# Performance work log

Hardware: AMD Instinct MI355X
Metric: run time of the kernel (lower is better)

Reference implementation:

```python
import jax, jax.numpy as jnp
import numpy as np

B, N, D, E = 4, 2048, 1024, 4
H = 4 * D  # expert hidden (mult=4)


def setup_inputs() -> dict:
    key = jax.random.key(0)
    ks = jax.random.split(key, 8)
    std = 0.02
    return {
        "x": jax.random.normal(ks[0], (B, N, D), jnp.float32),
        "W_slot": jax.random.normal(ks[1], (E * D, D), jnp.float32) * std,
        "u_slot": jax.random.normal(ks[2], (D,), jnp.float32),
        "sigma_slot": jnp.ones((1,), jnp.float32),
        "W1": jax.random.normal(ks[3], (E, H, D), jnp.float32) * std,
        "b1": jnp.zeros((E, H), jnp.float32),
        "u1": jax.random.normal(ks[4], (E, D), jnp.float32),
        "sig1": jnp.ones((E,), jnp.float32),
        "W2": jax.random.normal(ks[5], (E, D, H), jnp.float32) * std,
        "b2": jnp.zeros((E, D), jnp.float32),
        "u2": jax.random.normal(ks[6], (E, H), jnp.float32),
        "sig2": jnp.ones((E,), jnp.float32),
    }


def _sn_weight(W, u, sigma):
    # One power-iteration step (no_grad in torch -> stop_gradient), then
    # sigma_spec = v^T W u'; weight = W / sigma_spec * learnable sigma.
    v = W @ u
    v = jax.lax.stop_gradient(v / jnp.linalg.norm(v))
    u2 = W.T @ v
    u2 = jax.lax.stop_gradient(u2 / jnp.linalg.norm(u2))
    s = jnp.einsum('c,cd,d->', v, W, u2)
    return W * (sigma / s)


def reference(x, W_slot, u_slot, sigma_slot, W1, b1, u1, sig1, W2, b2, u2, sig2):
    b, n, d = x.shape
    e = W1.shape[0]
    s = n // e  # slots per expert; n divisible by e -> no padding, no mask

    # dynamic slot embeddings from consecutive-segment means
    Wsl = _sn_weight(W_slot, u_slot, sigma_slot[0])          # [e*d, d]
    xm = x.reshape(b, s, e, d).mean(axis=2)                   # [b, s, d]
    slot_embeds = (xm @ Wsl.T).reshape(b, s, e, d)
    slot_embeds = slot_embeds.transpose(0, 2, 1, 3)           # [b, e, s, d]

    logits = jnp.einsum('bnd,besd->bnes', x, slot_embeds)     # [b, n, e, s]
    dispatch = jax.nn.softmax(logits, axis=1)                 # softmax over n
    combine = jax.nn.softmax(logits.reshape(b, n, e * s), axis=-1)

    slots = jnp.einsum('bnd,bnes->ebsd', x, dispatch)         # [e, b, s, d]

    # per-expert FFN with spectral-normed weights (vectorized over experts)
    W1n = jax.vmap(_sn_weight)(W1, u1, sig1)                  # [e, H, d]
    W2n = jax.vmap(_sn_weight)(W2, u2, sig2)                  # [e, d, H]
    h = jax.nn.gelu(jnp.einsum('ebsd,ehd->ebsh', slots, W1n) + b1[:, None, None, :],
                    approximate=False)
    y = jnp.einsum('ebsh,edh->ebsd', h, W2n) + b2[:, None, None, :]

    out = y.transpose(1, 0, 2, 3).reshape(b, e * s, d)        # [b, e*s, d]
    return jnp.einsum('bsd,bns->bnd', out, combine)           # [b, n, d]
```

## Files before the change

### kernel.cpp

```cpp
#include <hip/hip_runtime.h>
#include <hip/hip_bf16.h>
#include <math.h>

constexpr int CB  = 4;
constexpr int CN  = 2048;
constexpr int CD  = 1024;
constexpr int CE  = 4;
constexpr int CS  = 512;
constexpr int CH  = 4096;
constexpr int CES = 2048;

typedef unsigned short u16;
typedef unsigned int   u32;
typedef __bf16 bf16x8 __attribute__((ext_vector_type(8)));
typedef float  f32x4  __attribute__((ext_vector_type(4)));

__device__ __forceinline__ u16 f2bf(float x) {
  u32 u = __float_as_uint(x);
  u = (u + 0x7FFF + ((u >> 16) & 1)) >> 16;
  return (u16)u;
}

__device__ __forceinline__ void gl2lds16(const void* g, void* l) {
  __builtin_amdgcn_global_load_lds(
      (const __attribute__((address_space(1))) void*)g,
      (__attribute__((address_space(3))) void*)l, 16, 0, 0);
}

__device__ __forceinline__ void xcd_swz(int& bx, int& by, int& bz) {
  u32 gx = gridDim.x, gy = gridDim.y;
  u32 w = blockIdx.x + gx * (blockIdx.y + gy * blockIdx.z);
  u32 nwg = gx * gy * gridDim.z;
  u32 q = nwg >> 3;
  u32 wg = (w & 7) * q + (w >> 3);
  bx = wg % gx;
  u32 r = wg / gx;
  by = r % gy;
  bz = r / gy;
}


__global__ __launch_bounds__(256) void gemv_rows_k(const float* __restrict__ W,
    const float* __restrict__ u, float* __restrict__ t1, int M, int K, int ustride) {
  int bi = blockIdx.y;
  int row = blockIdx.x * 4 + (threadIdx.x >> 6);
  int lane = threadIdx.x & 63;
  const float* Wr = W + ((long)bi * M + row) * K;
  const float* ub = u + (long)bi * ustride;
  float s = 0.f;
  for (int k = lane; k < K; k += 64) s += Wr[k] * ub[k];
#pragma unroll
  for (int off = 32; off; off >>= 1) s += __shfl_down(s, off, 64);
  if (lane == 0) t1[bi * M + row] = s;
}

__global__ __launch_bounds__(256) void gemv_cols_k(const float* __restrict__ W,
    const float* __restrict__ t1, float* __restrict__ t2,
    u16* __restrict__ bh, u16* __restrict__ bl, int M, int K) {
  int bi = blockIdx.z;
  int k = blockIdx.x * 256 + threadIdx.x;
  int m0 = blockIdx.y * 256;
  const float* Wb = W + (long)bi * M * K;
  const float* tb = t1 + bi * M;
  u16* bhb = bh + (long)bi * M * K;
  u16* blb = bl ? bl + (long)bi * M * K : nullptr;
  float s = 0.f;
#pragma unroll 4
  for (int m = 0; m < 256; m++) {
    long idx = (long)(m0 + m) * K + k;
    float w = Wb[idx];
    s += w * tb[m0 + m];
    u16 h = f2bf(w);
    bhb[idx] = h;
    if (blb) blb[idx] = f2bf(w - __uint_as_float((u32)h << 16));
  }
  atomicAdd(&t2[bi * K + k], s);
}

__global__ __launch_bounds__(256) void scale_all_k(
    const float* __restrict__ t1s, const float* __restrict__ t2s,
    const float* __restrict__ t1a, const float* __restrict__ t2a,
    const float* __restrict__ t1b, const float* __restrict__ t2b,
    const float* __restrict__ sigs, const float* __restrict__ sig1,
    const float* __restrict__ sig2, float* __restrict__ scales) {
  int bi = blockIdx.x;
  const float *t1, *t2; float sg; float* o; int M, K;
  if (bi == 0)      { t1 = t1s;                 t2 = t2s;                 sg = sigs[0];     o = scales + 0;      M = 4096; K = 1024; }
  else if (bi < 5)  { int e = bi - 1; t1 = t1a + e * 4096; t2 = t2a + e * 1024; sg = sig1[e]; o = scales + 1 + e; M = 4096; K = 1024; }
  else              { int e = bi - 5; t1 = t1b + e * 1024; t2 = t2b + e * 4096; sg = sig2[e]; o = scales + 5 + e; M = 1024; K = 4096; }
  int tid = threadIdx.x;
  __shared__ float red[256];
  float s1 = 0.f;
  for (int i = tid; i < M; i += 256) { float v = t1[i]; s1 += v * v; }
  red[tid] = s1; __syncthreads();
  for (int w = 128; w; w >>= 1) { if (tid < w) red[tid] += red[tid + w]; __syncthreads(); }
  float n1 = red[0]; __syncthreads();
  float s2 = 0.f;
  for (int i = tid; i < K; i += 256) { float v = t2[i]; s2 += v * v; }
  red[tid] = s2; __syncthreads();
  for (int w = 128; w; w >>= 1) { if (tid < w) red[tid] += red[tid + w]; __syncthreads(); }
  if (tid == 0) o[0] = sg * sqrtf(n1 / red[0]);
}

__global__ __launch_bounds__(256) void xsplit_fused_k(const float* __restrict__ x,
    u16* __restrict__ xh, u16* __restrict__ xl,
    u16* __restrict__ xmh, u16* __restrict__ xml) {
  int idx = blockIdx.x * 256 + threadIdx.x;
  int d8 = idx & (CD / 8 - 1);
  int si = (idx >> 7) & (CS - 1);
  int b  = idx >> 16;
  long rbase = ((long)(b * CN + si * 4)) * CD + d8 * 8;
  float vr[4][8];
#pragma unroll
  for (int r = 0; r < 4; r++) {
    float4 a = *(const float4*)(x + rbase + (long)r * CD);
    float4 c = *(const float4*)(x + rbase + (long)r * CD + 4);
    vr[r][0]=a.x; vr[r][1]=a.y; vr[r][2]=a.z; vr[r][3]=a.w;
    vr[r][4]=c.x; vr[r][5]=c.y; vr[r][6]=c.z; vr[r][7]=c.w;
  }
#pragma unroll
  for (int r = 0; r < 4; r++) {
    u16 oh[8], ol[8];
#pragma unroll
    for (int c = 0; c < 8; c++) {
      u16 h = f2bf(vr[r][c]);
      oh[c] = h;
      ol[c] = f2bf(vr[r][c] - __uint_as_float((u32)h << 16));
    }
    *(uint4*)(xh + rbase + (long)r * CD) = *(const uint4*)oh;
    *(uint4*)(xl + rbase + (long)r * CD) = *(const uint4*)ol;
  }
  long mbase = ((long)(b * CS + si)) * CD + d8 * 8;
  u16 oh[8], ol[8];
#pragma unroll
  for (int c = 0; c < 8; c++) {
    float v = 0.25f * (vr[0][c] + vr[1][c] + vr[2][c] + vr[3][c]);
    u16 h = f2bf(v);
    oh[c] = h;
    ol[c] = f2bf(v - __uint_as_float((u32)h << 16));
  }
  *(uint4*)(xmh + mbase) = *(const uint4*)oh;
  *(uint4*)(xml + mbase) = *(const uint4*)ol;
}

__global__ __launch_bounds__(256) void colstat_part_k(const float* __restrict__ lg,
    float* __restrict__ pmax, float* __restrict__ psum) {
  int es = blockIdx.x * 256 + threadIdx.x;
  int sl = blockIdx.y;
  int b  = blockIdx.z;
  const float* p = lg + ((long)(b * CN + sl * 256)) * CES + es;
  float m = -1e30f, s = 0.f;
  for (int i = 0; i < 256; i++) {
    float v = p[(long)i * CES];
    if (v > m) { s *= __expf(m - v); m = v; }
    s += __expf(v - m);
  }
  int o = (b * 8 + sl) * CES + es;
  pmax[o] = m; psum[o] = s;
}

__global__ __launch_bounds__(256) void colstat_comb_k(const float* __restrict__ pmax,
    const float* __restrict__ psum, float* __restrict__ cmax, float* __restrict__ csum) {
  int idx = blockIdx.x * 256 + threadIdx.x;
  int b = idx >> 11;
  int es = idx & (CES - 1);
  float m = -1e30f;
#pragma unroll
  for (int sl = 0; sl < 8; sl++) m = fmaxf(m, pmax[(b * 8 + sl) * CES + es]);
  float s = 0.f;
#pragma unroll
  for (int sl = 0; sl < 8; sl++)
    s += psum[(b * 8 + sl) * CES + es] * __expf(pmax[(b * 8 + sl) * CES + es] - m);
  cmax[idx] = m; csum[idx] = s;
}

__global__ __launch_bounds__(256) void rowcomb_k(const float* __restrict__ lg,
                                                 u16* __restrict__ outB) {
  __shared__ float red[8];
  long row = blockIdx.x;
  const float* p = lg + row * CES + threadIdx.x * 8;
  float4 a = *(const float4*)p;
  float4 b = *(const float4*)(p + 4);
  float v[8] = {a.x, a.y, a.z, a.w, b.x, b.y, b.z, b.w};
  float m = v[0];
#pragma unroll
  for (int c = 1; c < 8; c++) m = fmaxf(m, v[c]);
#pragma unroll
  for (int off = 32; off; off >>= 1) m = fmaxf(m, __shfl_xor(m, off, 64));
  int wv = threadIdx.x >> 6;
  if ((threadIdx.x & 63) == 0) red[wv] = m;
  __syncthreads();
  m = fmaxf(fmaxf(red[0], red[1]), fmaxf(red[2], red[3]));
  float s = 0.f;
#pragma unroll
  for (int c = 0; c < 8; c++) { v[c] = __expf(v[c] - m); s += v[c]; }
#pragma unroll
  for (int off = 32; off; off >>= 1) s += __shfl_xor(s, off, 64);
  if ((threadIdx.x & 63) == 0) red[4 + wv] = s;
  __syncthreads();
  float inv = 1.f / (red[4] + red[5] + red[6] + red[7]);
  u16 o[8];
#pragma unroll
  for (int c = 0; c < 8; c++) o[c] = f2bf(v[c] * inv);
  *(uint4*)(outB + row * CES + threadIdx.x * 8) = *(const uint4*)o;
}

__global__ __launch_bounds__(256) void tr_f2b_k(const float* __restrict__ in,
    u16* __restrict__ out, const float* __restrict__ sub, int R, int C, int expmode) {
  __shared__ u16 t[32][33];
  int z = blockIdx.z;
  long ibase = (long)z * R * C;
  int r0 = blockIdx.y * 32, c0 = blockIdx.x * 32;
  int tx = threadIdx.x & 31, ty = threadIdx.x >> 5;
  float cm = expmode ? sub[(long)z * C + c0 + tx] : 0.f;
  for (int rr = ty; rr < 32; rr += 8) {
    float v = in[ibase + (long)(r0 + rr) * C + c0 + tx];
    if (expmode) v = __expf(v - cm);
    t[tx][rr] = f2bf(v);
  }
  __syncthreads();
  for (int cc = ty; cc < 32; cc += 8)
    out[ibase + (long)(c0 + cc) * R + r0 + tx] = t[cc][tx];
}

struct MEpSESplit {
  u16* hi; u16* lo; const float* scale;
  __device__ void store(int z, int m, int n, float v) const {
    v *= scale[0];
    int b = m >> 9, si = m & 511, ei = n >> 10, di = n & 1023;
    long o = ((long)(b * CES + ei * 512 + si)) * CD + di;
    u16 h = f2bf(v);
    hi[o] = h;
    lo[o] = f2bf(v - __uint_as_float((u32)h << 16));
  }
};
struct MEpLogits {
  float* lg;
  __device__ void store(int b, int m, int n, float v) const {
    lg[((long)(b * CN + m)) * CES + n] = v;
  }
};
struct MEpSlots {
  u16* sb; const float* __restrict__ csum;
  __device__ void store(int b, int m, int n, float v) const {
    float inv = 1.f / csum[b * CES + m];
    int e = m >> 9, si = m & 511;
    sb[((long)(e * 2048 + b * 512 + si)) * CD + n] = f2bf(v * inv);
  }
};
struct MEpGelu {
  u16* h; const float* __restrict__ scales; const float* __restrict__ b1;
  __device__ void store(int e, int m, int n, float v) const {
    float xg = v * scales[1 + e] + b1[e * CH + n];
    float t = xg * (0.7978845608f + 0.0356774081f * xg * xg);
    float ex = __expf(2.f * t);
    float th = 1.f - 2.f / (ex + 1.f);
    float g = 0.5f * xg * (1.f + th);
    h[((long)(e * 2048 + m)) * CH + n] = f2bf(g);
  }
};
struct MEpYT {
  u16* ot; const float* __restrict__ scales; const float* __restrict__ b2;
  __device__ void store(int e, int m, int n, float v) const {
    int b = n >> 9, si = n & 511;
    ot[((long)(b * CD + m)) * CES + e * 512 + si] = f2bf(v * scales[5 + e] + b2[e * CD + m]);
  }
};
struct MEpOut {
  float* o;
  __device__ void store(int b, int m, int n, float v) const {
    o[((long)(b * CN + m)) * CD + n] = v;
  }
};


template <int BN, int BK, class EP>
__global__ __launch_bounds__(256) void mgemm_k(const u16* __restrict__ A, long Azs, int ldA,
                                               const u16* __restrict__ B, long Bzs, int ldB,
                                               EP ep, int K) {
  constexpr int BM = 128;
  constexpr int FI = 4;
  constexpr int FJ = BN / 32;
  constexpr int RPL = 512 / BK;
  constexpr int NGRP = (BM + BN) / RPL;
  constexpr int GPW = NGRP / 4;
  __shared__ __align__(16) u16 S[(BM + BN) * BK];
  int bx, by, bz;
  xcd_swz(bx, by, bz);
  const int tid = threadIdx.x;
  const int wid = tid >> 6, lane = tid & 63;
  const int m0 = by * BM, n0 = bx * BN;
  const u16* Az = A + (long)bz * Azs;
  const u16* Bz = B + (long)bz * Bzs;
  const int wr = wid >> 1, wc = wid & 1;
  const int lrow = lane / (BK / 8);
  const int lk   = (lane % (BK / 8)) * 8;

  f32x4 acc[FI][FJ];
  f32x4 zero = {0.f, 0.f, 0.f, 0.f};
#pragma unroll
  for (int i = 0; i < FI; i++)
#pragma unroll
    for (int j = 0; j < FJ; j++) acc[i][j] = zero;

  for (int k0 = 0; k0 < K; k0 += BK) {
#pragma unroll
    for (int g = 0; g < GPW; g++) {
      int grp = g * 4 + wid;
      int row = grp * RPL + lrow;
      const u16* src = (row < BM)
          ? Az + (long)(m0 + row) * ldA + k0 + lk
          : Bz + (long)(n0 + row - BM) * ldB + k0 + lk;
      gl2lds16(src, (char*)S + grp * 1024);
    }
    __syncthreads();
#pragma unroll
    for (int kk2 = 0; kk2 < BK / 32; kk2++) {
      bf16x8 af[FI], bfr[FJ];
#pragma unroll
      for (int i = 0; i < FI; i++) {
        int arow = wr * 64 + i * 16 + (lane & 15);
        af[i] = *(const bf16x8*)&S[arow * BK + kk2 * 32 + (lane >> 4) * 8];
      }
#pragma unroll
      for (int j = 0; j < FJ; j++) {
        int brow = BM + wc * (BN / 2) + j * 16 + (lane & 15);
        bfr[j] = *(const bf16x8*)&S[brow * BK + kk2 * 32 + (lane >> 4) * 8];
      }
#pragma unroll
      for (int i = 0; i < FI; i++)
#pragma unroll
        for (int j = 0; j < FJ; j++)
          acc[i][j] = __builtin_amdgcn_mfma_f32_16x16x32_bf16(af[i], bfr[j], acc[i][j], 0, 0, 0);
    }
    __syncthreads();
  }
#pragma unroll
  for (int i = 0; i < FI; i++) {
    int grow = m0 + wr * 64 + i * 16 + (lane >> 4) * 4;
#pragma unroll
    for (int j = 0; j < FJ; j++) {
      int gcol = n0 + wc * (BN / 2) + j * 16 + (lane & 15);
#pragma unroll
      for (int r = 0; r < 4; r++)
        ep.store(bz, grow + r, gcol, acc[i][j][r]);
    }
  }
}

template <class EP>
__global__ __launch_bounds__(256) void mgemm3_k(const u16* __restrict__ Ah,
                                                const u16* __restrict__ Al, long Azs, int ldA,
                                                const u16* __restrict__ Bh,
                                                const u16* __restrict__ Bl, long Bzs, int ldB,
                                                EP ep, int K) {
  constexpr int BK = 32;
  __shared__ __align__(16) u16 Ahs[128 * BK];
  __shared__ __align__(16) u16 Als[128 * BK];
  __shared__ __align__(16) u16 Bhs[128 * BK];
  __shared__ __align__(16) u16 Bls[128 * BK];
  int bx, by, bz;
  xcd_swz(bx, by, bz);
  const int tid = threadIdx.x;
  const int wid = tid >> 6, lane = tid & 63;
  const int m0 = by * 128, n0 = bx * 128;
  const u16* Ahz = Ah + (long)bz * Azs;
  const u16* Alz = Al + (long)bz * Azs;
  const u16* Bhz = Bh + (long)bz * Bzs;
  const u16* Blz = Bl + (long)bz * Bzs;
  const int wr = wid >> 1, wc = wid & 1;
  const int srow = lane >> 2;
  const int sk8  = (lane & 3) * 8;

  f32x4 acc[4][4];
  f32x4 zero = {0.f, 0.f, 0.f, 0.f};
#pragma unroll
  for (int i = 0; i < 4; i++)
#pragma unroll
    for (int j = 0; j < 4; j++) acc[i][j] = zero;

  for (int k0 = 0; k0 < K; k0 += BK) {
#pragma unroll
    for (int i = 0; i < 2; i++) {
      int chunk = i * 4 + wid;
      int r = chunk * 16 + srow;
      long ao = (long)(m0 + r) * ldA + k0 + sk8;
      long bo = (long)(n0 + r) * ldB + k0 + sk8;
      gl2lds16(Ahz + ao, (char*)Ahs + chunk * 1024);
      gl2lds16(Alz + ao, (char*)Als + chunk * 1024);
      gl2lds16(Bhz + bo, (char*)Bhs + chunk * 1024);
      gl2lds16(Blz + bo, (char*)Bls + chunk * 1024);
    }
    __syncthreads();
    bf16x8 ah[4], al[4], bh[4], bl[4];
#pragma unroll
    for (int i = 0; i < 4; i++) {
      int arow = wr * 64 + i * 16 + (lane & 15);
      int aoff = arow * BK + (lane >> 4) * 8;
      ah[i] = *(const bf16x8*)&Ahs[aoff];
      al[i] = *(const bf16x8*)&Als[aoff];
      int brow = wc * 64 + i * 16 + (lane & 15);
      int boff = brow * BK + (lane >> 4) * 8;
      bh[i] = *(const bf16x8*)&Bhs[boff];
      bl[i] = *(const bf16x8*)&Bls[boff];
    }
#pragma unroll
    for (int i = 0; i < 4; i++)
#pragma unroll
      for (int j = 0; j < 4; j++) {
        acc[i][j] = __builtin_amdgcn_mfma_f32_16x16x32_bf16(ah[i], bh[j], acc[i][j], 0, 0, 0);
        acc[i][j] = __builtin_amdgcn_mfma_f32_16x16x32_bf16(al[i], bh[j], acc[i][j], 0, 0, 0);
        acc[i][j] = __builtin_amdgcn_mfma_f32_16x16x32_bf16(ah[i], bl[j], acc[i][j], 0, 0, 0);
      }
    __syncthreads();
  }
#pragma unroll
  for (int i = 0; i < 4; i++) {
    int grow = m0 + wr * 64 + i * 16 + (lane >> 4) * 4;
#pragma unroll
    for (int j = 0; j < 4; j++) {
      int gcol = n0 + wc * 64 + j * 16 + (lane & 15);
#pragma unroll
      for (int r = 0; r < 4; r++)
        ep.store(bz, grow + r, gcol, acc[i][j][r]);
    }
  }
}

extern "C" void kernel_launch(void* const* d_in, const int* in_sizes, int n_in,
                              void* d_out, int out_size, void* d_ws, size_t ws_size,
                              hipStream_t stream) {
  const float* x          = (const float*)d_in[0];
  const float* W_slot     = (const float*)d_in[1];
  const float* u_slot     = (const float*)d_in[2];
  const float* sigma_slot = (const float*)d_in[3];
  const float* W1         = (const float*)d_in[4];
  const float* b1         = (const float*)d_in[5];
  const float* u1         = (const float*)d_in[6];
  const float* sig1       = (const float*)d_in[7];
  const float* W2         = (const float*)d_in[8];
  const float* b2         = (const float*)d_in[9];
  const float* u2         = (const float*)d_in[10];
  const float* sig2       = (const float*)d_in[11];
  float* out = (float*)d_out;

  char* ws = (char*)d_ws;
  size_t off = 0;
  auto alloc = [&](size_t bytes) -> char* {
    char* p = ws + off;
    off += (bytes + 255) & ~(size_t)255;
    return p;
  };
  float* t1s = (float*)alloc(4096 * 4);
  float* t1a = (float*)alloc(4 * 4096 * 4);
  float* t1b = (float*)alloc(4 * 1024 * 4);
  float* t2s = (float*)alloc(1024 * 4);
  float* t2a = (float*)alloc(4 * 1024 * 4);
  float* t2b = (float*)alloc(4 * 4096 * 4);
  float* scales = (float*)alloc(16 * 4);
  float* pmax   = (float*)alloc((size_t)CB * 8 * CES * 4);
  float* psum   = (float*)alloc((size_t)CB * 8 * CES * 4);
  float* cmax   = (float*)alloc((size_t)CB * CES * 4);
  float* csum   = (float*)alloc((size_t)CB * CES * 4);
  char* regAB   = alloc((size_t)CB * CN * CD * 2 * 2);
  char* regBB   = alloc((size_t)CB * CES * CD * 2 * 2);
  char* regL    = alloc((size_t)CB * CN * CES * 4);
  char* regS    = alloc((size_t)CE * CB * CS * CD * 2);
  u16* W1b      = (u16*)alloc((size_t)CE * CH * CD * 2);
  u16* W2b      = (u16*)alloc((size_t)CE * CD * CH * 2);

  u16*   xh      = (u16*)regAB;
  u16*   xl      = (u16*)(regAB + (size_t)CB * CN * CD * 2);
  u16*   dispT   = (u16*)regAB;
  u16*   combineB= (u16*)regAB;
  u16*   seh     = (u16*)regBB;
  u16*   sel     = (u16*)(regBB + (size_t)CB * CES * CD * 2);
  u16*   xT      = (u16*)regBB;
  float* logits  = (float*)regL;
  u16*   hbuf    = (u16*)regL;
  u16*   xmh     = (u16*)regL;
  u16*   xml     = (u16*)(regL + (size_t)CB * CS * CD * 2);
  u16*   wslh    = (u16*)(regL + (size_t)2 * CB * CS * CD * 2);
  u16*   wsll    = (u16*)(regL + (size_t)2 * CB * CS * CD * 2 + (size_t)CE * CD * CD * 2);
  u16*   slotsB  = (u16*)regS;
  u16*   outbufT = (u16*)regS;

  hipMemsetAsync(t2s, 0, (size_t)((char*)t2b - (char*)t2s) + 4 * 4096 * 4, stream);

  gemv_rows_k<<<dim3(4096 / 4, 1), 256, 0, stream>>>(W_slot, u_slot, t1s, 4096, 1024, 0);
  gemv_rows_k<<<dim3(4096 / 4, 4), 256, 0, stream>>>(W1, u1, t1a, CH, CD, CD);
  gemv_rows_k<<<dim3(1024 / 4, 4), 256, 0, stream>>>(W2, u2, t1b, CD, CH, CH);
  gemv_cols_k<<<dim3(1024 / 256, 4096 / 256, 1), 256, 0, stream>>>(W_slot, t1s, t2s, wslh, wsll, 4096, 1024);
  gemv_cols_k<<<dim3(1024 / 256, 4096 / 256, 4), 256, 0, stream>>>(W1, t1a, t2a, W1b, nullptr, CH, CD);
  gemv_cols_k<<<dim3(4096 / 256, 1024 / 256, 4), 256, 0, stream>>>(W2, t1b, t2b, W2b, nullptr, CD, CH);
  scale_all_k<<<9, 256, 0, stream>>>(t1s, t2s, t1a, t2a, t1b, t2b,
                                     sigma_slot, sig1, sig2, scales);

  xsplit_fused_k<<<(CB * CS * (CD / 8)) / 256, 256, 0, stream>>>(x, xh, xl, xmh, xml);

  mgemm3_k<<<dim3(4096 / 128, 2048 / 128, 1), 256, 0, stream>>>(
      xmh, xml, 0L, CD, wslh, wsll, 0L, CD, MEpSESplit{seh, sel, scales}, CD);

  mgemm3_k<<<dim3(CES / 128, CN / 128, CB), 256, 0, stream>>>(
      xh, xl, (long)CN * CD, CD, seh, sel, (long)CES * CD, CD,
      MEpLogits{logits}, CD);

  colstat_part_k<<<dim3(CES / 256, 8, CB), 256, 0, stream>>>(logits, pmax, psum);
  colstat_comb_k<<<(CB * CES) / 256, 256, 0, stream>>>(pmax, psum, cmax, csum);

  tr_f2b_k<<<dim3(CES / 32, CN / 32, CB), 256, 0, stream>>>(logits, dispT, cmax, CN, CES, 1);
  tr_f2b_k<<<dim3(CD / 32, CN / 32, CB), 256, 0, stream>>>(x, xT, nullptr, CN, CD, 0);

  mgemm_k<64, 64><<<dim3(CD / 64, CES / 128, CB), 256, 0, stream>>>(
      dispT, (long)CES * CN, CN, xT, (long)CD * CN, CN, MEpSlots{slotsB, csum}, CN);

  rowcomb_k<<<CB * CN, 256, 0, stream>>>(logits, combineB);

  mgemm_k<128, 64><<<dim3(CH / 128, 2048 / 128, CE), 256, 0, stream>>>(
      slotsB, (long)2048 * CD, CD, W1b, (long)CH * CD, CD, MEpGelu{hbuf, scales, b1}, CD);

  mgemm_k<64, 64><<<dim3(2048 / 64, CD / 128, CE), 256, 0, stream>>>(
      W2b, (long)CD * CH, CH, hbuf, (long)2048 * CH, CH, MEpYT{outbufT, scales, b2}, CH);

  mgemm_k<64, 64><<<dim3(CD / 64, CN / 128, CB), 256, 0, stream>>>(
      combineB, (long)CN * CES, CES, outbufT, (long)CD * CES, CES, MEpOut{out}, CES);

  (void)in_sizes; (void)n_in; (void)out_size; (void)ws_size;
}
```

Measured before the change: 899.8 us.

## Fuse column softmax partial stats into logits GEMM epilogue, retune FFN1 tile

Computes per-column max and sum-exp partials for the dispatch softmax inside the logits GEMM epilogue, using register reductions, shuffles and shared memory per 128-row tile. This removes the separate colstat_part kernel, which re-read the full fp32 logits tensor column-wise. The combine step now merges 16 partials instead of 8. It also changes the FFN1 GEMM tile template parameter from 64 to 32, at the cost of two extra barriers and some register pressure in the logits GEMM.

```diff
diff --git a/kernel.cpp b/kernel.cpp
--- a/kernel.cpp
+++ b/kernel.cpp
@@ -143,22 +143,6 @@
   *(uint4*)(xml + mbase) = *(const uint4*)ol;
 }
 
-__global__ __launch_bounds__(256) void colstat_part_k(const float* __restrict__ lg,
-    float* __restrict__ pmax, float* __restrict__ psum) {
-  int es = blockIdx.x * 256 + threadIdx.x;
-  int sl = blockIdx.y;
-  int b  = blockIdx.z;
-  const float* p = lg + ((long)(b * CN + sl * 256)) * CES + es;
-  float m = -1e30f, s = 0.f;
-  for (int i = 0; i < 256; i++) {
-    float v = p[(long)i * CES];
-    if (v > m) { s *= __expf(m - v); m = v; }
-    s += __expf(v - m);
-  }
-  int o = (b * 8 + sl) * CES + es;
-  pmax[o] = m; psum[o] = s;
-}
-
 __global__ __launch_bounds__(256) void colstat_comb_k(const float* __restrict__ pmax,
     const float* __restrict__ psum, float* __restrict__ cmax, float* __restrict__ csum) {
   int idx = blockIdx.x * 256 + threadIdx.x;
@@ -166,11 +150,11 @@
   int es = idx & (CES - 1);
   float m = -1e30f;
 #pragma unroll
-  for (int sl = 0; sl < 8; sl++) m = fmaxf(m, pmax[(b * 8 + sl) * CES + es]);
+  for (int sl = 0; sl < 16; sl++) m = fmaxf(m, pmax[(b * 16 + sl) * CES + es]);
   float s = 0.f;
 #pragma unroll
-  for (int sl = 0; sl < 8; sl++)
-    s += psum[(b * 8 + sl) * CES + es] * __expf(pmax[(b * 8 + sl) * CES + es] - m);
+  for (int sl = 0; sl < 16; sl++)
+    s += psum[(b * 16 + sl) * CES + es] * __expf(pmax[(b * 16 + sl) * CES + es] - m);
   cmax[idx] = m; csum[idx] = s;
 }
 
@@ -348,12 +332,14 @@
   }
 }
 
-template <class EP>
+template <bool CSTAT, class EP>
 __global__ __launch_bounds__(256) void mgemm3_k(const u16* __restrict__ Ah,
                                                 const u16* __restrict__ Al, long Azs, int ldA,
                                                 const u16* __restrict__ Bh,
                                                 const u16* __restrict__ Bl, long Bzs, int ldB,
-                                                EP ep, int K) {
+                                                EP ep, int K,
+                                                float* __restrict__ pmax,
+                                                float* __restrict__ psum) {
   constexpr int BK = 32;
   __shared__ __align__(16) u16 Ahs[128 * BK];
   __shared__ __align__(16) u16 Als[128 * BK];
@@ -425,6 +411,55 @@
         ep.store(bz, grow + r, gcol, acc[i][j][r]);
     }
   }
+
+  if constexpr (CSTAT) {
+    __shared__ float cred[2][128];
+    __shared__ float sred[2][128];
+    float cmv[4], lsum[4];
+#pragma unroll
+    for (int j = 0; j < 4; j++) {
+      float m = acc[0][j][0];
+#pragma unroll
+      for (int i = 0; i < 4; i++)
+#pragma unroll
+        for (int r = 0; r < 4; r++) m = fmaxf(m, acc[i][j][r]);
+      m = fmaxf(m, __shfl_xor(m, 16, 64));
+      m = fmaxf(m, __shfl_xor(m, 32, 64));
+      cmv[j] = m;
+    }
+    if (lane < 16) {
+#pragma unroll
+      for (int j = 0; j < 4; j++) cred[wr][wc * 64 + j * 16 + lane] = cmv[j];
+    }
+    __syncthreads();
+#pragma unroll
+    for (int j = 0; j < 4; j++) {
+      int c = wc * 64 + j * 16 + (lane & 15);
+      float cm = fmaxf(cred[0][c], cred[1][c]);
+      float s = 0.f;
+#pragma unroll
+      for (int i = 0; i < 4; i++)
+#pragma unroll
+        for (int r = 0; r < 4; r++) s += __expf(acc[i][j][r] - cm);
+      s += __shfl_xor(s, 16, 64);
+      s += __shfl_xor(s, 32, 64);
+      cmv[j] = cm; lsum[j] = s;
+    }
+    if (lane < 16) {
+#pragma unroll
+      for (int j = 0; j < 4; j++) sred[wr][wc * 64 + j * 16 + lane] = lsum[j];
+    }
+    __syncthreads();
+    if (wr == 0 && lane < 16) {
+      long sb = ((long)bz * 16 + by) * CES + n0;
+#pragma unroll
+      for (int j = 0; j < 4; j++) {
+        int c = wc * 64 + j * 16 + lane;
+        pmax[sb + c] = cmv[j];
+        psum[sb + c] = sred[0][c] + sred[1][c];
+      }
+    }
+  }
 }
 
 extern "C" void kernel_launch(void* const* d_in, const int* in_sizes, int n_in,
@@ -458,8 +493,8 @@
   float* t2a = (float*)alloc(4 * 1024 * 4);
   float* t2b = (float*)alloc(4 * 4096 * 4);
   float* scales = (float*)alloc(16 * 4);
-  float* pmax   = (float*)alloc((size_t)CB * 8 * CES * 4);
-  float* psum   = (float*)alloc((size_t)CB * 8 * CES * 4);
+  float* pmax   = (float*)alloc((size_t)CB * 16 * CES * 4);
+  float* psum   = (float*)alloc((size_t)CB * 16 * CES * 4);
   float* cmax   = (float*)alloc((size_t)CB * CES * 4);
   float* csum   = (float*)alloc((size_t)CB * CES * 4);
   char* regAB   = alloc((size_t)CB * CN * CD * 2 * 2);
@@ -498,14 +533,14 @@
 
   xsplit_fused_k<<<(CB * CS * (CD / 8)) / 256, 256, 0, stream>>>(x, xh, xl, xmh, xml);
 
-  mgemm3_k<<<dim3(4096 / 128, 2048 / 128, 1), 256, 0, stream>>>(
-      xmh, xml, 0L, CD, wslh, wsll, 0L, CD, MEpSESplit{seh, sel, scales}, CD);
-
-  mgemm3_k<<<dim3(CES / 128, CN / 128, CB), 256, 0, stream>>>(
+  mgemm3_k<false><<<dim3(4096 / 128, 2048 / 128, 1), 256, 0, stream>>>(
+      xmh, xml, 0L, CD, wslh, wsll, 0L, CD, MEpSESplit{seh, sel, scales}, CD,
+      nullptr, nullptr);
+
+  mgemm3_k<true><<<dim3(CES / 128, CN / 128, CB), 256, 0, stream>>>(
       xh, xl, (long)CN * CD, CD, seh, sel, (long)CES * CD, CD,
-      MEpLogits{logits}, CD);
-
-  colstat_part_k<<<dim3(CES / 256, 8, CB), 256, 0, stream>>>(logits, pmax, psum);
+      MEpLogits{logits}, CD, pmax, psum);
+
   colstat_comb_k<<<(CB * CES) / 256, 256, 0, stream>>>(pmax, psum, cmax, csum);
 
   tr_f2b_k<<<dim3(CES / 32, CN / 32, CB), 256, 0, stream>>>(logits, dispT, cmax, CN, CES, 1);
@@ -516,7 +551,7 @@
 
   rowcomb_k<<<CB * CN, 256, 0, stream>>>(logits, combineB);
 
-  mgemm_k<128, 64><<<dim3(CH / 128, 2048 / 128, CE), 256, 0, stream>>>(
+  mgemm_k<128, 32><<<dim3(CH / 128, 2048 / 128, CE), 256, 0, stream>>>(
       slotsB, (long)2048 * CD, CD, W1b, (long)CH * CD, CD, MEpGelu{hbuf, scales, b1}, CD);
 
   mgemm_k<64, 64><<<dim3(2048 / 64, CD / 128, CE), 256, 0, stream>>>(
```

Result: faster. 865.1 us (-3.8%).
